# Kernel tuning notes

Measured on AMD Instinct MI355X. Metric: run time of the kernel, lower is better.

## Reference

```python
import jax, jax.numpy as jnp
import numpy as np

D = 1024
HEADS = 16
HEAD_DIM = D // HEADS


def setup_inputs() -> dict:
    key = jax.random.key(0)
    k1, k2, k3, k4 = jax.random.split(key, 4)
    B, L = 2, 2048
    x = jax.random.normal(k1, (B, L, D), dtype=jnp.float32)
    mask = jnp.ones((B, L), dtype=jnp.float32)
    # qkv: Linear(D, 3D, bias=False); H: Linear(D, D) with bias
    W_qkv = jax.random.normal(k2, (D, 3 * D), dtype=jnp.float32) / np.sqrt(D)
    W_h = jax.random.normal(k3, (D, D), dtype=jnp.float32) / np.sqrt(D)
    b_h = jax.random.normal(k4, (D,), dtype=jnp.float32) * 0.01
    return {"x": x, "mask": mask, "W_qkv": W_qkv, "W_h": W_h, "b_h": b_h}


def reference(x, mask, W_qkv, W_h, b_h):
    B, L, _ = x.shape
    qkv = x @ W_qkv  # [B, L, 3D]
    Q, K, V = jnp.split(qkv, 3, axis=-1)
    Q = Q.reshape(B, L, HEADS, HEAD_DIM)
    K = K.reshape(B, L, HEADS, HEAD_DIM)
    V = V.reshape(B, L, HEADS, HEAD_DIM)
    scores = jnp.einsum('bqhd,bkhd->bhqk', Q, K)
    # outer-product mask, applied BEFORE the 1/sqrt(D) scaling (as in source)
    true_mask = jnp.einsum('bq,bk->bqk', mask, mask)[:, None, :, :]  # [B,1,L,L]
    scores = jnp.where(true_mask == 0, jnp.float32(-100000.0), scores)
    attn = jax.nn.softmax(scores / np.sqrt(D).astype(np.float32), axis=-1)
    attn_out = jnp.einsum('bhqv,bvhd->bqhd', attn, V)
    output = attn_out.reshape(B, L, D) @ W_h + b_h
    return (output, attn)
```

## Files before the change

### kernel.cpp

```cpp
#include <hip/hip_runtime.h>

typedef __attribute__((ext_vector_type(4))) float f32x4;
typedef __attribute__((ext_vector_type(8))) short bf16x8;
typedef __attribute__((ext_vector_type(8))) unsigned short us8;
typedef __attribute__((ext_vector_type(4))) unsigned short us4;
typedef __attribute__((ext_vector_type(4))) float fl4;

static __device__ __forceinline__ unsigned short f2bf(float f) {
  union { float f; unsigned int u; } v; v.f = f;
  unsigned int u = v.u;
  return (unsigned short)((u + 0x7FFFu + ((u >> 16) & 1u)) >> 16);
}

#define MFMA16(a, b, c) __builtin_amdgcn_mfma_f32_16x16x32_bf16((a), (b), (c), 0, 0, 0)

__global__ __launch_bounds__(256) void convert_x(const float* __restrict__ in,
                                                 unsigned short* __restrict__ out, int n) {
  int i = (blockIdx.x * 256 + threadIdx.x) * 4;
  if (i >= n) return;
  fl4 v = *(const fl4*)&in[i];
  us4 o;
  o[0] = f2bf(v[0]); o[1] = f2bf(v[1]); o[2] = f2bf(v[2]); o[3] = f2bf(v[3]);
  *(us4*)&out[i] = o;
}

__global__ __launch_bounds__(256) void transpose_w(const float* __restrict__ in,
                                                   unsigned short* __restrict__ out,
                                                   int R, int C) {
  __shared__ float t[32][33];
  int bc = blockIdx.x * 32;
  int br = blockIdx.y * 32;
  int tx = threadIdx.x & 31, ty = threadIdx.x >> 5;
#pragma unroll
  for (int i = 0; i < 32; i += 8)
    t[ty + i][tx] = in[(br + ty + i) * C + bc + tx];
  __syncthreads();
#pragma unroll
  for (int i = 0; i < 32; i += 8)
    out[(bc + ty + i) * R + br + tx] = f2bf(t[tx][ty + i]);
}

__global__ __launch_bounds__(256) void transpose_v(const unsigned short* __restrict__ V,
                                                   unsigned short* __restrict__ Vt) {
  __shared__ unsigned short t[64][65];
  int bh = blockIdx.y;
  int q0 = blockIdx.x * 64;
  int tid = threadIdx.x;
#pragma unroll
  for (int i = 0; i < 16; i++) {
    int idx = tid + i * 256;
    int r = idx >> 6, c = idx & 63;
    t[r][c] = V[((size_t)bh * 2048 + q0 + r) * 64 + c];
  }
  __syncthreads();
#pragma unroll
  for (int i = 0; i < 16; i++) {
    int idx = tid + i * 256;
    int d = idx >> 6, q = idx & 63;
    Vt[((size_t)bh * 64 + d) * 2048 + q0 + q] = t[q][d];
  }
}

__global__ __launch_bounds__(256) void gemm_qkv(const unsigned short* __restrict__ X,
                                                const unsigned short* __restrict__ Bt,
                                                unsigned short* __restrict__ Qw,
                                                unsigned short* __restrict__ Kw,
                                                unsigned short* __restrict__ Vw) {
  __shared__ unsigned short As[128 * 32];
  __shared__ unsigned short Bs[128 * 32];
  const int tid = threadIdx.x;
  const int wave = tid >> 6, lane = tid & 63;
  const int quad = lane >> 4, ln = lane & 15;
  const int m0 = blockIdx.x * 128, n0 = blockIdx.y * 128;
  const int wr = (wave >> 1) * 64, wc = (wave & 1) * 64;
  const int srow = tid >> 2, soff = (tid & 3) << 3;
  f32x4 acc[4][4] = {};
  const unsigned short* Ag = X + (m0 + srow) * 1024 + soff;
  const unsigned short* Bg = Bt + (n0 + srow) * 1024 + soff;
  for (int k0 = 0; k0 < 1024; k0 += 32) {
    us8 a0 = *(const us8*)(Ag + k0);
    us8 a1 = *(const us8*)(Ag + 64 * 1024 + k0);
    us8 b0 = *(const us8*)(Bg + k0);
    us8 b1 = *(const us8*)(Bg + 64 * 1024 + k0);
    __syncthreads();
    *(us8*)&As[srow * 32 + soff] = a0;
    *(us8*)&As[(srow + 64) * 32 + soff] = a1;
    *(us8*)&Bs[srow * 32 + soff] = b0;
    *(us8*)&Bs[(srow + 64) * 32 + soff] = b1;
    __syncthreads();
    bf16x8 af[4], bfr[4];
#pragma unroll
    for (int i = 0; i < 4; i++) af[i] = *(const bf16x8*)&As[(wr + i * 16 + ln) * 32 + quad * 8];
#pragma unroll
    for (int j = 0; j < 4; j++) bfr[j] = *(const bf16x8*)&Bs[(wc + j * 16 + ln) * 32 + quad * 8];
#pragma unroll
    for (int i = 0; i < 4; i++)
#pragma unroll
      for (int j = 0; j < 4; j++)
        acc[i][j] = MFMA16(af[i], bfr[j], acc[i][j]);
  }
#pragma unroll
  for (int j = 0; j < 4; j++) {
    int col = n0 + wc + j * 16 + ln;
    int part = col >> 10;
    int h = (col >> 6) & 15;
    int d = col & 63;
    unsigned short* dst = (part == 0) ? Qw : ((part == 1) ? Kw : Vw);
#pragma unroll
    for (int i = 0; i < 4; i++)
#pragma unroll
      for (int r = 0; r < 4; r++) {
        int row = m0 + wr + i * 16 + quad * 4 + r;
        int idx = ((((row >> 11) << 4) + h) * 2048 + (row & 2047)) * 64 + d;
        dst[idx] = f2bf(acc[i][j][r]);
      }
  }
}

__global__ __launch_bounds__(256) void attn_fused(const unsigned short* __restrict__ Qw,
                                                  const unsigned short* __restrict__ Kw,
                                                  const unsigned short* __restrict__ Vt,
                                                  const float* __restrict__ mask,
                                                  float* __restrict__ attn,
                                                  unsigned short* __restrict__ AO) {
  __shared__ unsigned short Qs[64 * 64];
  __shared__ unsigned short Ks[64 * 64];
  __shared__ unsigned short Vs[64 * 64];
  __shared__ unsigned short Ps[4][16 * 64];
  __shared__ float mQ[64];
  __shared__ float mK[64];
  const int tid = threadIdx.x;
  const int wave = tid >> 6, lane = tid & 63;
  const int quad = lane >> 4, ln = lane & 15;
  const int bh = blockIdx.y, b = bh >> 4, h = bh & 15;
  const int q0 = blockIdx.x * 64;
  const float scale = 0.03125f;
  const int c0 = tid, r0 = c0 >> 3, o0 = (c0 & 7) << 3;
  const int c1 = tid + 256, r1 = c1 >> 3, o1 = (c1 & 7) << 3;
  const unsigned short* Qg = Qw + (size_t)bh * 2048 * 64;
  const unsigned short* Kg = Kw + (size_t)bh * 2048 * 64;
  const unsigned short* Vg = Vt + (size_t)bh * 64 * 2048;

  *(us8*)&Qs[r0 * 64 + o0] = *(const us8*)&Qg[(q0 + r0) * 64 + o0];
  *(us8*)&Qs[r1 * 64 + o1] = *(const us8*)&Qg[(q0 + r1) * 64 + o1];
  if (tid < 64) mQ[tid] = mask[b * 2048 + q0 + tid];
  __syncthreads();

  const int qrb = wave * 16 + quad * 4;
  float mq[4];
#pragma unroll
  for (int r = 0; r < 4; r++) mq[r] = mQ[qrb + r];
  const bf16x8 aq0 = *(const bf16x8*)&Qs[(wave * 16 + ln) * 64 + quad * 8];
  const bf16x8 aq1 = *(const bf16x8*)&Qs[(wave * 16 + ln) * 64 + 32 + quad * 8];

  float mrun[4], lrun[4];
#pragma unroll
  for (int r = 0; r < 4; r++) { mrun[r] = -3.0e38f; lrun[r] = 0.0f; }

  for (int kt = 0; kt < 32; kt++) {
    const int k0 = kt * 64;
    us8 ka = *(const us8*)&Kg[(k0 + r0) * 64 + o0];
    us8 kb = *(const us8*)&Kg[(k0 + r1) * 64 + o1];
    float mkv = 0.0f;
    if (tid < 64) mkv = mask[b * 2048 + k0 + tid];
    __syncthreads();
    *(us8*)&Ks[r0 * 64 + o0] = ka;
    *(us8*)&Ks[r1 * 64 + o1] = kb;
    if (tid < 64) mK[tid] = mkv;
    __syncthreads();
    f32x4 s[4] = {};
#pragma unroll
    for (int nt = 0; nt < 4; nt++) {
      bf16x8 kb0 = *(const bf16x8*)&Ks[(nt * 16 + ln) * 64 + quad * 8];
      bf16x8 kb1 = *(const bf16x8*)&Ks[(nt * 16 + ln) * 64 + 32 + quad * 8];
      s[nt] = MFMA16(aq0, kb0, s[nt]);
      s[nt] = MFMA16(aq1, kb1, s[nt]);
    }
    float mkl[4];
#pragma unroll
    for (int nt = 0; nt < 4; nt++) mkl[nt] = mK[nt * 16 + ln];
    float lg[4][4], lmax[4];
#pragma unroll
    for (int r = 0; r < 4; r++) lmax[r] = -3.0e38f;
#pragma unroll
    for (int nt = 0; nt < 4; nt++)
#pragma unroll
      for (int r = 0; r < 4; r++) {
        float lgv = (mq[r] * mkl[nt] == 0.0f) ? -3125.0f : s[nt][r] * scale;
        lg[nt][r] = lgv;
        lmax[r] = fmaxf(lmax[r], lgv);
      }
#pragma unroll
    for (int off = 1; off < 16; off <<= 1)
#pragma unroll
      for (int r = 0; r < 4; r++) lmax[r] = fmaxf(lmax[r], __shfl_xor(lmax[r], off, 64));
    float ps[4] = {0.0f, 0.0f, 0.0f, 0.0f};
#pragma unroll
    for (int r = 0; r < 4; r++) {
      float mnew = fmaxf(mrun[r], lmax[r]);
      lrun[r] *= __expf(mrun[r] - mnew);
      mrun[r] = mnew;
    }
#pragma unroll
    for (int nt = 0; nt < 4; nt++)
#pragma unroll
      for (int r = 0; r < 4; r++) ps[r] += __expf(lg[nt][r] - mrun[r]);
#pragma unroll
    for (int off = 1; off < 16; off <<= 1)
#pragma unroll
      for (int r = 0; r < 4; r++) ps[r] += __shfl_xor(ps[r], off, 64);
#pragma unroll
    for (int r = 0; r < 4; r++) lrun[r] += ps[r];
  }

  float invl[4];
#pragma unroll
  for (int r = 0; r < 4; r++) invl[r] = 1.0f / lrun[r];
  float* arow[4];
#pragma unroll
  for (int r = 0; r < 4; r++) arow[r] = attn + ((size_t)bh * 2048 + (q0 + qrb + r)) * 2048;

  f32x4 o[4] = {};
  for (int kt = 0; kt < 32; kt++) {
    const int k0 = kt * 64;
    us8 ka = *(const us8*)&Kg[(k0 + r0) * 64 + o0];
    us8 kb = *(const us8*)&Kg[(k0 + r1) * 64 + o1];
    us8 va = *(const us8*)&Vg[r0 * 2048 + k0 + o0];
    us8 vb = *(const us8*)&Vg[r1 * 2048 + k0 + o1];
    float mkv = 0.0f;
    if (tid < 64) mkv = mask[b * 2048 + k0 + tid];
    __syncthreads();
    *(us8*)&Ks[r0 * 64 + o0] = ka;
    *(us8*)&Ks[r1 * 64 + o1] = kb;
    *(us8*)&Vs[r0 * 64 + o0] = va;
    *(us8*)&Vs[r1 * 64 + o1] = vb;
    if (tid < 64) mK[tid] = mkv;
    __syncthreads();
    f32x4 s[4] = {};
#pragma unroll
    for (int nt = 0; nt < 4; nt++) {
      bf16x8 kb0 = *(const bf16x8*)&Ks[(nt * 16 + ln) * 64 + quad * 8];
      bf16x8 kb1 = *(const bf16x8*)&Ks[(nt * 16 + ln) * 64 + 32 + quad * 8];
      s[nt] = MFMA16(aq0, kb0, s[nt]);
      s[nt] = MFMA16(aq1, kb1, s[nt]);
    }
    float mkl[4];
#pragma unroll
    for (int nt = 0; nt < 4; nt++) mkl[nt] = mK[nt * 16 + ln];
#pragma unroll
    for (int nt = 0; nt < 4; nt++)
#pragma unroll
      for (int r = 0; r < 4; r++) {
        float lgv = (mq[r] * mkl[nt] == 0.0f) ? -3125.0f : s[nt][r] * scale;
        float p = __expf(lgv - mrun[r]) * invl[r];
        arow[r][k0 + nt * 16 + ln] = p;
        Ps[wave][(quad * 4 + r) * 64 + nt * 16 + ln] = f2bf(p);
      }
    bf16x8 pa0 = *(const bf16x8*)&Ps[wave][ln * 64 + quad * 8];
    bf16x8 pa1 = *(const bf16x8*)&Ps[wave][ln * 64 + 32 + quad * 8];
#pragma unroll
    for (int nt = 0; nt < 4; nt++) {
      bf16x8 vb0 = *(const bf16x8*)&Vs[(nt * 16 + ln) * 64 + quad * 8];
      bf16x8 vb1 = *(const bf16x8*)&Vs[(nt * 16 + ln) * 64 + 32 + quad * 8];
      o[nt] = MFMA16(pa0, vb0, o[nt]);
      o[nt] = MFMA16(pa1, vb1, o[nt]);
    }
  }
#pragma unroll
  for (int nt = 0; nt < 4; nt++)
#pragma unroll
    for (int r = 0; r < 4; r++) {
      int token = b * 2048 + q0 + qrb + r;
      AO[(size_t)token * 1024 + h * 64 + nt * 16 + ln] = f2bf(o[nt][r]);
    }
}

__global__ __launch_bounds__(256) void gemm_out(const unsigned short* __restrict__ A,
                                                const unsigned short* __restrict__ Bt,
                                                const float* __restrict__ bias,
                                                float* __restrict__ out) {
  __shared__ unsigned short As[128 * 32];
  __shared__ unsigned short Bs[128 * 32];
  const int tid = threadIdx.x;
  const int wave = tid >> 6, lane = tid & 63;
  const int quad = lane >> 4, ln = lane & 15;
  const int m0 = blockIdx.x * 128, n0 = blockIdx.y * 128;
  const int wr = (wave >> 1) * 64, wc = (wave & 1) * 64;
  const int srow = tid >> 2, soff = (tid & 3) << 3;
  f32x4 acc[4][4] = {};
  const unsigned short* Ag = A + (m0 + srow) * 1024 + soff;
  const unsigned short* Bg = Bt + (n0 + srow) * 1024 + soff;
  for (int k0 = 0; k0 < 1024; k0 += 32) {
    us8 a0 = *(const us8*)(Ag + k0);
    us8 a1 = *(const us8*)(Ag + 64 * 1024 + k0);
    us8 b0 = *(const us8*)(Bg + k0);
    us8 b1 = *(const us8*)(Bg + 64 * 1024 + k0);
    __syncthreads();
    *(us8*)&As[srow * 32 + soff] = a0;
    *(us8*)&As[(srow + 64) * 32 + soff] = a1;
    *(us8*)&Bs[srow * 32 + soff] = b0;
    *(us8*)&Bs[(srow + 64) * 32 + soff] = b1;
    __syncthreads();
    bf16x8 af[4], bfr[4];
#pragma unroll
    for (int i = 0; i < 4; i++) af[i] = *(const bf16x8*)&As[(wr + i * 16 + ln) * 32 + quad * 8];
#pragma unroll
    for (int j = 0; j < 4; j++) bfr[j] = *(const bf16x8*)&Bs[(wc + j * 16 + ln) * 32 + quad * 8];
#pragma unroll
    for (int i = 0; i < 4; i++)
#pragma unroll
      for (int j = 0; j < 4; j++)
        acc[i][j] = MFMA16(af[i], bfr[j], acc[i][j]);
  }
#pragma unroll
  for (int j = 0; j < 4; j++) {
    int col = n0 + wc + j * 16 + ln;
    float bv = bias[col];
#pragma unroll
    for (int i = 0; i < 4; i++)
#pragma unroll
      for (int r = 0; r < 4; r++) {
        int row = m0 + wr + i * 16 + quad * 4 + r;
        out[(size_t)row * 1024 + col] = acc[i][j][r] + bv;
      }
  }
}

extern "C" void kernel_launch(void* const* d_in, const int* in_sizes, int n_in,
                              void* d_out, int out_size, void* d_ws, size_t ws_size,
                              hipStream_t stream) {
  const float* x = (const float*)d_in[0];
  const float* mask = (const float*)d_in[1];
  const float* Wqkv = (const float*)d_in[2];
  const float* Wh = (const float*)d_in[3];
  const float* bh = (const float*)d_in[4];
  float* out = (float*)d_out;
  float* attn = out + 4194304;

  unsigned short* ws = (unsigned short*)d_ws;
  unsigned short* Xbf   = ws;
  unsigned short* WqkvT = ws + 4194304;
  unsigned short* WhT   = ws + 7340032;
  unsigned short* Qw    = ws + 8388608;
  unsigned short* Kw    = ws + 12582912;
  unsigned short* Vw    = ws + 16777216;
  unsigned short* Vtw   = ws + 20971520;
  unsigned short* AO    = ws + 25165824;

  convert_x<<<dim3(4096), dim3(256), 0, stream>>>(x, Xbf, 4194304);
  transpose_w<<<dim3(96, 32), dim3(256), 0, stream>>>(Wqkv, WqkvT, 1024, 3072);
  transpose_w<<<dim3(32, 32), dim3(256), 0, stream>>>(Wh, WhT, 1024, 1024);
  gemm_qkv<<<dim3(32, 24), dim3(256), 0, stream>>>(Xbf, WqkvT, Qw, Kw, Vw);
  transpose_v<<<dim3(32, 32), dim3(256), 0, stream>>>(Vw, Vtw);
  attn_fused<<<dim3(32, 32), dim3(256), 0, stream>>>(Qw, Kw, Vtw, mask, attn, AO);
  gemm_out<<<dim3(32, 8), dim3(256), 0, stream>>>(AO, WhT, bh, out);
}
```

Before: 836.0 us.

## Use direct global-to-LDS loads in GEMMs, pad attention LDS, prefetch K/V, drop max tracking

Result: faster. 753.6 us (-9.9%).

```diff
diff --git a/kernel.cpp b/kernel.cpp
--- a/kernel.cpp
+++ b/kernel.cpp
@@ -13,6 +13,10 @@
 }
 
 #define MFMA16(a, b, c) __builtin_amdgcn_mfma_f32_16x16x32_bf16((a), (b), (c), 0, 0, 0)
+
+#define GLL16(g, l) __builtin_amdgcn_global_load_lds(                       \
+    (const __attribute__((address_space(1))) void*)(g),                     \
+    (__attribute__((address_space(3))) void*)(l), 16, 0, 0)
 
 __global__ __launch_bounds__(256) void convert_x(const float* __restrict__ in,
                                                  unsigned short* __restrict__ out, int n) {
@@ -66,8 +70,8 @@
                                                 unsigned short* __restrict__ Qw,
                                                 unsigned short* __restrict__ Kw,
                                                 unsigned short* __restrict__ Vw) {
-  __shared__ unsigned short As[128 * 32];
-  __shared__ unsigned short Bs[128 * 32];
+  __shared__ __align__(16) unsigned short As[128 * 32];
+  __shared__ __align__(16) unsigned short Bs[128 * 32];
   const int tid = threadIdx.x;
   const int wave = tid >> 6, lane = tid & 63;
   const int quad = lane >> 4, ln = lane & 15;
@@ -77,16 +81,16 @@
   f32x4 acc[4][4] = {};
   const unsigned short* Ag = X + (m0 + srow) * 1024 + soff;
   const unsigned short* Bg = Bt + (n0 + srow) * 1024 + soff;
+  unsigned short* asw0 = &As[wave * 512];
+  unsigned short* asw1 = &As[2048 + wave * 512];
+  unsigned short* bsw0 = &Bs[wave * 512];
+  unsigned short* bsw1 = &Bs[2048 + wave * 512];
   for (int k0 = 0; k0 < 1024; k0 += 32) {
-    us8 a0 = *(const us8*)(Ag + k0);
-    us8 a1 = *(const us8*)(Ag + 64 * 1024 + k0);
-    us8 b0 = *(const us8*)(Bg + k0);
-    us8 b1 = *(const us8*)(Bg + 64 * 1024 + k0);
-    __syncthreads();
-    *(us8*)&As[srow * 32 + soff] = a0;
-    *(us8*)&As[(srow + 64) * 32 + soff] = a1;
-    *(us8*)&Bs[srow * 32 + soff] = b0;
-    *(us8*)&Bs[(srow + 64) * 32 + soff] = b1;
+    __syncthreads();
+    GLL16(Ag + k0, asw0);
+    GLL16(Ag + 65536 + k0, asw1);
+    GLL16(Bg + k0, bsw0);
+    GLL16(Bg + 65536 + k0, bsw1);
     __syncthreads();
     bf16x8 af[4], bfr[4];
 #pragma unroll
@@ -117,16 +121,17 @@
   }
 }
 
+#define STR 72
 __global__ __launch_bounds__(256) void attn_fused(const unsigned short* __restrict__ Qw,
                                                   const unsigned short* __restrict__ Kw,
                                                   const unsigned short* __restrict__ Vt,
                                                   const float* __restrict__ mask,
                                                   float* __restrict__ attn,
                                                   unsigned short* __restrict__ AO) {
-  __shared__ unsigned short Qs[64 * 64];
-  __shared__ unsigned short Ks[64 * 64];
-  __shared__ unsigned short Vs[64 * 64];
-  __shared__ unsigned short Ps[4][16 * 64];
+  __shared__ __align__(16) unsigned short Qs[64 * STR];
+  __shared__ __align__(16) unsigned short Ks[64 * STR];
+  __shared__ __align__(16) unsigned short Vs[64 * STR];
+  __shared__ __align__(16) unsigned short Ps[4][16 * STR];
   __shared__ float mQ[64];
   __shared__ float mK[64];
   const int tid = threadIdx.x;
@@ -135,14 +140,13 @@
   const int bh = blockIdx.y, b = bh >> 4, h = bh & 15;
   const int q0 = blockIdx.x * 64;
   const float scale = 0.03125f;
-  const int c0 = tid, r0 = c0 >> 3, o0 = (c0 & 7) << 3;
-  const int c1 = tid + 256, r1 = c1 >> 3, o1 = (c1 & 7) << 3;
+  const int r0 = tid >> 3, o0 = (tid & 7) << 3;
   const unsigned short* Qg = Qw + (size_t)bh * 2048 * 64;
   const unsigned short* Kg = Kw + (size_t)bh * 2048 * 64;
   const unsigned short* Vg = Vt + (size_t)bh * 64 * 2048;
 
-  *(us8*)&Qs[r0 * 64 + o0] = *(const us8*)&Qg[(q0 + r0) * 64 + o0];
-  *(us8*)&Qs[r1 * 64 + o1] = *(const us8*)&Qg[(q0 + r1) * 64 + o1];
+  *(us8*)&Qs[r0 * STR + o0] = *(const us8*)&Qg[(q0 + r0) * 64 + o0];
+  *(us8*)&Qs[(r0 + 32) * STR + o0] = *(const us8*)&Qg[(q0 + r0 + 32) * 64 + o0];
   if (tid < 64) mQ[tid] = mask[b * 2048 + q0 + tid];
   __syncthreads();
 
@@ -150,118 +154,109 @@
   float mq[4];
 #pragma unroll
   for (int r = 0; r < 4; r++) mq[r] = mQ[qrb + r];
-  const bf16x8 aq0 = *(const bf16x8*)&Qs[(wave * 16 + ln) * 64 + quad * 8];
-  const bf16x8 aq1 = *(const bf16x8*)&Qs[(wave * 16 + ln) * 64 + 32 + quad * 8];
-
-  float mrun[4], lrun[4];
-#pragma unroll
-  for (int r = 0; r < 4; r++) { mrun[r] = -3.0e38f; lrun[r] = 0.0f; }
-
+  const bf16x8 aq0 = *(const bf16x8*)&Qs[(wave * 16 + ln) * STR + quad * 8];
+  const bf16x8 aq1 = *(const bf16x8*)&Qs[(wave * 16 + ln) * STR + 32 + quad * 8];
+
+  float lrun[4] = {0.0f, 0.0f, 0.0f, 0.0f};
+
+  us8 ka = *(const us8*)&Kg[r0 * 64 + o0];
+  us8 kb = *(const us8*)&Kg[(r0 + 32) * 64 + o0];
+  float mkv = (tid < 64) ? mask[b * 2048 + tid] : 0.0f;
+  for (int kt = 0; kt < 32; kt++) {
+    __syncthreads();
+    *(us8*)&Ks[r0 * STR + o0] = ka;
+    *(us8*)&Ks[(r0 + 32) * STR + o0] = kb;
+    if (tid < 64) mK[tid] = mkv;
+    __syncthreads();
+    if (kt < 31) {
+      const int k0n = (kt + 1) * 64;
+      ka = *(const us8*)&Kg[(k0n + r0) * 64 + o0];
+      kb = *(const us8*)&Kg[(k0n + r0 + 32) * 64 + o0];
+      if (tid < 64) mkv = mask[b * 2048 + k0n + tid];
+    }
+    f32x4 s[4] = {};
+#pragma unroll
+    for (int nt = 0; nt < 4; nt++) {
+      bf16x8 kb0 = *(const bf16x8*)&Ks[(nt * 16 + ln) * STR + quad * 8];
+      bf16x8 kb1 = *(const bf16x8*)&Ks[(nt * 16 + ln) * STR + 32 + quad * 8];
+      s[nt] = MFMA16(aq0, kb0, s[nt]);
+      s[nt] = MFMA16(aq1, kb1, s[nt]);
+    }
+    float mkl[4];
+#pragma unroll
+    for (int nt = 0; nt < 4; nt++) mkl[nt] = mK[nt * 16 + ln];
+    float ps[4] = {0.0f, 0.0f, 0.0f, 0.0f};
+#pragma unroll
+    for (int nt = 0; nt < 4; nt++)
+#pragma unroll
+      for (int r = 0; r < 4; r++) {
+        float lgv = (mq[r] * mkl[nt] == 0.0f) ? -3125.0f : s[nt][r] * scale;
+        ps[r] += __expf(lgv);
+      }
+#pragma unroll
+    for (int off = 1; off < 16; off <<= 1)
+#pragma unroll
+      for (int r = 0; r < 4; r++) ps[r] += __shfl_xor(ps[r], off, 64);
+#pragma unroll
+    for (int r = 0; r < 4; r++) lrun[r] += ps[r];
+  }
+
+  float invl[4];
+#pragma unroll
+  for (int r = 0; r < 4; r++) invl[r] = 1.0f / lrun[r];
+  float* arow[4];
+#pragma unroll
+  for (int r = 0; r < 4; r++) arow[r] = attn + ((size_t)bh * 2048 + (q0 + qrb + r)) * 2048;
+
+  f32x4 o[4] = {};
+  ka = *(const us8*)&Kg[r0 * 64 + o0];
+  kb = *(const us8*)&Kg[(r0 + 32) * 64 + o0];
+  us8 va = *(const us8*)&Vg[r0 * 2048 + o0];
+  us8 vb = *(const us8*)&Vg[(r0 + 32) * 2048 + o0];
+  mkv = (tid < 64) ? mask[b * 2048 + tid] : 0.0f;
   for (int kt = 0; kt < 32; kt++) {
     const int k0 = kt * 64;
-    us8 ka = *(const us8*)&Kg[(k0 + r0) * 64 + o0];
-    us8 kb = *(const us8*)&Kg[(k0 + r1) * 64 + o1];
-    float mkv = 0.0f;
-    if (tid < 64) mkv = mask[b * 2048 + k0 + tid];
-    __syncthreads();
-    *(us8*)&Ks[r0 * 64 + o0] = ka;
-    *(us8*)&Ks[r1 * 64 + o1] = kb;
+    __syncthreads();
+    *(us8*)&Ks[r0 * STR + o0] = ka;
+    *(us8*)&Ks[(r0 + 32) * STR + o0] = kb;
+    *(us8*)&Vs[r0 * STR + o0] = va;
+    *(us8*)&Vs[(r0 + 32) * STR + o0] = vb;
     if (tid < 64) mK[tid] = mkv;
     __syncthreads();
+    if (kt < 31) {
+      const int k0n = k0 + 64;
+      ka = *(const us8*)&Kg[(k0n + r0) * 64 + o0];
+      kb = *(const us8*)&Kg[(k0n + r0 + 32) * 64 + o0];
+      va = *(const us8*)&Vg[r0 * 2048 + k0n + o0];
+      vb = *(const us8*)&Vg[(r0 + 32) * 2048 + k0n + o0];
+      if (tid < 64) mkv = mask[b * 2048 + k0n + tid];
+    }
     f32x4 s[4] = {};
 #pragma unroll
     for (int nt = 0; nt < 4; nt++) {
-      bf16x8 kb0 = *(const bf16x8*)&Ks[(nt * 16 + ln) * 64 + quad * 8];
-      bf16x8 kb1 = *(const bf16x8*)&Ks[(nt * 16 + ln) * 64 + 32 + quad * 8];
+      bf16x8 kb0 = *(const bf16x8*)&Ks[(nt * 16 + ln) * STR + quad * 8];
+      bf16x8 kb1 = *(const bf16x8*)&Ks[(nt * 16 + ln) * STR + 32 + quad * 8];
       s[nt] = MFMA16(aq0, kb0, s[nt]);
       s[nt] = MFMA16(aq1, kb1, s[nt]);
     }
     float mkl[4];
 #pragma unroll
     for (int nt = 0; nt < 4; nt++) mkl[nt] = mK[nt * 16 + ln];
-    float lg[4][4], lmax[4];
-#pragma unroll
-    for (int r = 0; r < 4; r++) lmax[r] = -3.0e38f;
 #pragma unroll
     for (int nt = 0; nt < 4; nt++)
 #pragma unroll
       for (int r = 0; r < 4; r++) {
         float lgv = (mq[r] * mkl[nt] == 0.0f) ? -3125.0f : s[nt][r] * scale;
-        lg[nt][r] = lgv;
-        lmax[r] = fmaxf(lmax[r], lgv);
+        float p = __expf(lgv) * invl[r];
+        arow[r][k0 + nt * 16 + ln] = p;
+        Ps[wave][(quad * 4 + r) * STR + nt * 16 + ln] = f2bf(p);
       }
-#pragma unroll
-    for (int off = 1; off < 16; off <<= 1)
-#pragma unroll
-      for (int r = 0; r < 4; r++) lmax[r] = fmaxf(lmax[r], __shfl_xor(lmax[r], off, 64));
-    float ps[4] = {0.0f, 0.0f, 0.0f, 0.0f};
-#pragma unroll
-    for (int r = 0; r < 4; r++) {
-      float mnew = fmaxf(mrun[r], lmax[r]);
-      lrun[r] *= __expf(mrun[r] - mnew);
-      mrun[r] = mnew;
-    }
-#pragma unroll
-    for (int nt = 0; nt < 4; nt++)
-#pragma unroll
-      for (int r = 0; r < 4; r++) ps[r] += __expf(lg[nt][r] - mrun[r]);
-#pragma unroll
-    for (int off = 1; off < 16; off <<= 1)
-#pragma unroll
-      for (int r = 0; r < 4; r++) ps[r] += __shfl_xor(ps[r], off, 64);
-#pragma unroll
-    for (int r = 0; r < 4; r++) lrun[r] += ps[r];
-  }
-
-  float invl[4];
-#pragma unroll
-  for (int r = 0; r < 4; r++) invl[r] = 1.0f / lrun[r];
-  float* arow[4];
-#pragma unroll
-  for (int r = 0; r < 4; r++) arow[r] = attn + ((size_t)bh * 2048 + (q0 + qrb + r)) * 2048;
-
-  f32x4 o[4] = {};
-  for (int kt = 0; kt < 32; kt++) {
-    const int k0 = kt * 64;
-    us8 ka = *(const us8*)&Kg[(k0 + r0) * 64 + o0];
-    us8 kb = *(const us8*)&Kg[(k0 + r1) * 64 + o1];
-    us8 va = *(const us8*)&Vg[r0 * 2048 + k0 + o0];
-    us8 vb = *(const us8*)&Vg[r1 * 2048 + k0 + o1];
-    float mkv = 0.0f;
-    if (tid < 64) mkv = mask[b * 2048 + k0 + tid];
-    __syncthreads();
-    *(us8*)&Ks[r0 * 64 + o0] = ka;
-    *(us8*)&Ks[r1 * 64 + o1] = kb;
-    *(us8*)&Vs[r0 * 64 + o0] = va;
-    *(us8*)&Vs[r1 * 64 + o1] = vb;
-    if (tid < 64) mK[tid] = mkv;
-    __syncthreads();
-    f32x4 s[4] = {};
+    bf16x8 pa0 = *(const bf16x8*)&Ps[wave][ln * STR + quad * 8];
+    bf16x8 pa1 = *(const bf16x8*)&Ps[wave][ln * STR + 32 + quad * 8];
 #pragma unroll
     for (int nt = 0; nt < 4; nt++) {
-      bf16x8 kb0 = *(const bf16x8*)&Ks[(nt * 16 + ln) * 64 + quad * 8];
-      bf16x8 kb1 = *(const bf16x8*)&Ks[(nt * 16 + ln) * 64 + 32 + quad * 8];
-      s[nt] = MFMA16(aq0, kb0, s[nt]);
-      s[nt] = MFMA16(aq1, kb1, s[nt]);
-    }
-    float mkl[4];
-#pragma unroll
-    for (int nt = 0; nt < 4; nt++) mkl[nt] = mK[nt * 16 + ln];
-#pragma unroll
-    for (int nt = 0; nt < 4; nt++)
-#pragma unroll
-      for (int r = 0; r < 4; r++) {
-        float lgv = (mq[r] * mkl[nt] == 0.0f) ? -3125.0f : s[nt][r] * scale;
-        float p = __expf(lgv - mrun[r]) * invl[r];
-        arow[r][k0 + nt * 16 + ln] = p;
-        Ps[wave][(quad * 4 + r) * 64 + nt * 16 + ln] = f2bf(p);
-      }
-    bf16x8 pa0 = *(const bf16x8*)&Ps[wave][ln * 64 + quad * 8];
-    bf16x8 pa1 = *(const bf16x8*)&Ps[wave][ln * 64 + 32 + quad * 8];
-#pragma unroll
-    for (int nt = 0; nt < 4; nt++) {
-      bf16x8 vb0 = *(const bf16x8*)&Vs[(nt * 16 + ln) * 64 + quad * 8];
-      bf16x8 vb1 = *(const bf16x8*)&Vs[(nt * 16 + ln) * 64 + 32 + quad * 8];
+      bf16x8 vb0 = *(const bf16x8*)&Vs[(nt * 16 + ln) * STR + quad * 8];
+      bf16x8 vb1 = *(const bf16x8*)&Vs[(nt * 16 + ln) * STR + 32 + quad * 8];
       o[nt] = MFMA16(pa0, vb0, o[nt]);
       o[nt] = MFMA16(pa1, vb1, o[nt]);
     }
@@ -279,8 +274,8 @@
                                                 const unsigned short* __restrict__ Bt,
                                                 const float* __restrict__ bias,
                                                 float* __restrict__ out) {
-  __shared__ unsigned short As[128 * 32];
-  __shared__ unsigned short Bs[128 * 32];
+  __shared__ __align__(16) unsigned short As[128 * 32];
+  __shared__ __align__(16) unsigned short Bs[128 * 32];
   const int tid = threadIdx.x;
   const int wave = tid >> 6, lane = tid & 63;
   const int quad = lane >> 4, ln = lane & 15;
@@ -290,16 +285,16 @@
   f32x4 acc[4][4] = {};
   const unsigned short* Ag = A + (m0 + srow) * 1024 + soff;
   const unsigned short* Bg = Bt + (n0 + srow) * 1024 + soff;
+  unsigned short* asw0 = &As[wave * 512];
+  unsigned short* asw1 = &As[2048 + wave * 512];
+  unsigned short* bsw0 = &Bs[wave * 512];
+  unsigned short* bsw1 = &Bs[2048 + wave * 512];
   for (int k0 = 0; k0 < 1024; k0 += 32) {
-    us8 a0 = *(const us8*)(Ag + k0);
-    us8 a1 = *(const us8*)(Ag + 64 * 1024 + k0);
-    us8 b0 = *(const us8*)(Bg + k0);
-    us8 b1 = *(const us8*)(Bg + 64 * 1024 + k0);
-    __syncthreads();
-    *(us8*)&As[srow * 32 + soff] = a0;
-    *(us8*)&As[(srow + 64) * 32 + soff] = a1;
-    *(us8*)&Bs[srow * 32 + soff] = b0;
-    *(us8*)&Bs[(srow + 64) * 32 + soff] = b1;
+    __syncthreads();
+    GLL16(Ag + k0, asw0);
+    GLL16(Ag + 65536 + k0, asw1);
+    GLL16(Bg + k0, bsw0);
+    GLL16(Bg + 65536 + k0, bsw1);
     __syncthreads();
     bf16x8 af[4], bfr[4];
 #pragma unroll
```
